# Kernel optimization log

Hardware: AMD Instinct MI355X
Metric: run time of the kernel (lower is better)

The kernel has to match this reference:

```python
import jax, jax.numpy as jnp
import numpy as np

BN_EPS = 1e-5

def setup_inputs() -> dict:
    key = jax.random.key(0)
    ks = jax.random.split(key, 6)
    B, C, N = 8, 256, 4096
    da = C // 4
    return {
        "x": jax.random.normal(ks[0], (B, C, N), dtype=jnp.float32),
        "Wq": jax.random.normal(ks[1], (da, C), dtype=jnp.float32) * (C ** -0.5),
        "Wk": jax.random.normal(ks[2], (da, C), dtype=jnp.float32) * (C ** -0.5),
        "Wv": jax.random.normal(ks[3], (C, C), dtype=jnp.float32) * (C ** -0.5),
        "Wp": jax.random.normal(ks[4], (C, C), dtype=jnp.float32) * (C ** -0.5),
        "bn_gamma": jnp.ones((C,), dtype=jnp.float32),
        "bn_beta": jnp.zeros((C,), dtype=jnp.float32),
        "bn_mean": jnp.zeros((C,), dtype=jnp.float32),
        "bn_var": jnp.ones((C,), dtype=jnp.float32),
    }

def reference(x, Wq, Wk, Wv, Wp, bn_gamma, bn_beta, bn_mean, bn_var):
    # x: [B, C, N]; 1x1 Conv1d == channel matmul
    q = jnp.einsum('bcn,dc->bnd', x, Wq)          # [B, N, da]
    k = jnp.einsum('bcn,dc->bdn', x, Wk)          # [B, da, N]
    v = jnp.einsum('bcn,dc->bnd', x, Wv)          # [B, N, C]
    energy = jnp.einsum('bnd,bdm->bnm', q, k)     # [B, N, N]
    # offset-attention double normalization: softmax over dim=1 (rows), then L1 over dim=-1
    attn = jax.nn.softmax(energy, axis=1)
    attn = attn / (1e-9 + attn.sum(axis=-1, keepdims=True))
    fsa = jnp.einsum('bnm,bmc->bcn', attn, v)     # [B, C, N]
    y = x - fsa
    h = jnp.einsum('bcn,dc->bdn', y, Wp)          # 1x1 conv of LBR
    # BatchNorm1d (inference-mode with running stats)
    inv = bn_gamma / jnp.sqrt(bn_var + BN_EPS)
    h = h * inv[None, :, None] + (bn_beta - bn_mean * inv)[None, :, None]
    return jax.nn.relu(h) + x
```

## Files before the change

kernel.cpp:

```cpp
#include <hip/hip_runtime.h>
#include <math.h>

#define BD 8
#define CD 256
#define ND 4096
#define DA 64

typedef __attribute__((ext_vector_type(8))) short short8v;
typedef __attribute__((ext_vector_type(4))) float float4v;

static __device__ __forceinline__ float4v mfma16(short8v a, short8v b, float4v c) {
  return __builtin_amdgcn_mfma_f32_16x16x32_bf16(a, b, c, 0, 0, 0);
}
static __device__ __forceinline__ unsigned short f2bf(float f) {
  union { float f; unsigned int u; } v; v.f = f;
  return (unsigned short)((v.u + 0x7fffu + ((v.u >> 16) & 1u)) >> 16);
}
static __device__ __forceinline__ float bf2f(unsigned short h) {
  union { unsigned int u; float f; } v; v.u = (unsigned int)h << 16;
  return v.f;
}
static __device__ __forceinline__ int sw(int row, int c8) {
  return row * 64 + (((c8) ^ (row & 7)) << 3);
}
typedef const __attribute__((address_space(1))) unsigned int g_u32;
typedef __attribute__((address_space(3))) unsigned int l_u32;
static __device__ __forceinline__ void gld16(const void* g, void* l) {
  __builtin_amdgcn_global_load_lds((g_u32*)g, (l_u32*)l, 16, 0, 0);
}

__global__ __launch_bounds__(256) void k_prep(const float* __restrict__ x,
                                              unsigned short* __restrict__ xTh,
                                              unsigned short* __restrict__ xTl) {
  const int n0 = blockIdx.x * 64, c0 = blockIdx.y * 64, b = blockIdx.z;
  __shared__ float Xs[64][68];
  const int tid = threadIdx.x;
  const int r0 = tid >> 4, col4 = (tid & 15) * 4;
#pragma unroll
  for (int j = 0; j < 4; ++j) {
    int r = r0 + j * 16;
    *(float4*)&Xs[r][col4] =
        *(const float4*)&x[((size_t)(b * CD + c0 + r)) * ND + n0 + col4];
  }
  __syncthreads();
  const int n = tid >> 2, cg = (tid & 3) * 16;
  unsigned short h[16], l[16];
#pragma unroll
  for (int j = 0; j < 16; ++j) {
    float v = Xs[cg + j][n];
    h[j] = f2bf(v);
    l[j] = f2bf(v - bf2f(h[j]));
  }
  size_t o = ((size_t)b * ND + n0 + n) * CD + c0 + cg;
#pragma unroll
  for (int j = 0; j < 4; ++j) {
    *(ushort4*)&xTh[o + j * 4] = *(ushort4*)&h[j * 4];
    *(ushort4*)&xTl[o + j * 4] = *(ushort4*)&l[j * 4];
  }
}

__global__ void k_prepW(const float* __restrict__ Wq, const float* __restrict__ Wk,
                        const float* __restrict__ Wv, const float* __restrict__ Wp,
                        unsigned short* Wch, unsigned short* Wcl,
                        unsigned short* Wph, unsigned short* Wpl) {
  int i = blockIdx.x * 256 + threadIdx.x;
  int row = i >> 6, c4 = (i & 63) * 4;
  const float* src; unsigned short *dh, *dl; int r, drow;
  if (row < 64)       { src = Wq; r = row;       dh = Wch; dl = Wcl; drow = row; }
  else if (row < 128) { src = Wk; r = row - 64;  dh = Wch; dl = Wcl; drow = row; }
  else if (row < 384) { src = Wv; r = row - 128; dh = Wch; dl = Wcl; drow = row; }
  else                { src = Wp; r = row - 384; dh = Wph; dl = Wpl; drow = row - 384; }
  float4 f = *(const float4*)&src[(size_t)r * 256 + c4];
  ushort4 hh, ll;
  hh.x = f2bf(f.x); hh.y = f2bf(f.y); hh.z = f2bf(f.z); hh.w = f2bf(f.w);
  ll.x = f2bf(f.x - bf2f(hh.x)); ll.y = f2bf(f.y - bf2f(hh.y));
  ll.z = f2bf(f.z - bf2f(hh.z)); ll.w = f2bf(f.w - bf2f(hh.w));
  *(ushort4*)&dh[(size_t)drow * 256 + c4] = hh;
  *(ushort4*)&dl[(size_t)drow * 256 + c4] = ll;
}

__global__ __launch_bounds__(512) void k_proj(
    const unsigned short* __restrict__ xTh, const unsigned short* __restrict__ xTl,
    const unsigned short* __restrict__ Wch, const unsigned short* __restrict__ Wcl,
    unsigned short* __restrict__ qh, unsigned short* __restrict__ kh,
    unsigned short* __restrict__ kl, unsigned short* __restrict__ vT) {
  const int n0 = blockIdx.x * 128, b = blockIdx.y;
  const int tid = threadIdx.x, w = tid >> 6, lane = tid & 63, lq = lane & 15,
            quad = lane >> 4;
  __shared__ __align__(16) unsigned short xs[2][2][128][40];
  float4v O[24];
#pragma unroll
  for (int t = 0; t < 24; ++t) O[t] = (float4v){0.f, 0.f, 0.f, 0.f};

  const int srow = tid >> 2, sc4 = tid & 3;
  uint4 rh, rl;
  auto load_slice = [&](int ks) {
    size_t a = ((size_t)b * ND + n0 + srow) * CD + ks * 32 + sc4 * 8;
    rh = *(const uint4*)(xTh + a);
    rl = *(const uint4*)(xTl + a);
  };
  auto write_slice = [&](int buf) {
    *(uint4*)&xs[buf][0][srow][sc4 * 8] = rh;
    *(uint4*)&xs[buf][1][srow][sc4 * 8] = rl;
  };
  load_slice(0); write_slice(0);
#pragma unroll 1
  for (int ks = 0; ks < 8; ++ks) {
    __syncthreads();
    if (ks < 7) load_slice(ks + 1);
    short8v bxh = *(const short8v*)&xs[ks & 1][0][w * 16 + lq][quad * 8];
    short8v bxl = *(const short8v*)&xs[ks & 1][1][w * 16 + lq][quad * 8];
#pragma unroll
    for (int t = 0; t < 24; ++t) {
      size_t a = (size_t)(t * 16 + lq) * CD + ks * 32 + quad * 8;
      short8v awh = *(const short8v*)(Wch + a);
      short8v awl = *(const short8v*)(Wcl + a);
      O[t] = mfma16(awh, bxh, O[t]);
      O[t] = mfma16(awl, bxh, O[t]);
      O[t] = mfma16(awh, bxl, O[t]);
    }
    if (ks < 7) write_slice((ks + 1) & 1);
  }
  const int n = n0 + w * 16 + lq;
#pragma unroll
  for (int t = 0; t < 24; ++t) {
    if (t < 4) {
      ushort4 hh;
      hh.x = f2bf(O[t][0]); hh.y = f2bf(O[t][1]);
      hh.z = f2bf(O[t][2]); hh.w = f2bf(O[t][3]);
      *(ushort4*)&qh[((size_t)b * ND + n) * DA + t * 16 + quad * 4] = hh;
    } else if (t < 8) {
      ushort4 hh, ll;
      hh.x = f2bf(O[t][0]); hh.y = f2bf(O[t][1]);
      hh.z = f2bf(O[t][2]); hh.w = f2bf(O[t][3]);
      ll.x = f2bf(O[t][0] - bf2f(hh.x)); ll.y = f2bf(O[t][1] - bf2f(hh.y));
      ll.z = f2bf(O[t][2] - bf2f(hh.z)); ll.w = f2bf(O[t][3] - bf2f(hh.w));
      size_t o = ((size_t)b * ND + n) * DA + (t - 4) * 16 + quad * 4;
      *(ushort4*)&kh[o] = hh;
      *(ushort4*)&kl[o] = ll;
    } else {
#pragma unroll
      for (int r = 0; r < 4; ++r) {
        int c = (t - 8) * 16 + quad * 4 + r;
        vT[((size_t)b * CD + c) * ND + n] = f2bf(O[t][r]);
      }
    }
  }
}

__global__ __launch_bounds__(512, 4) void k_colsum(
    const unsigned short* __restrict__ qh, const unsigned short* __restrict__ khp,
    const unsigned short* __restrict__ klp, float* __restrict__ Dp) {
  const int bid = blockIdx.x, b = bid & 7, half = (bid >> 3) & 1,
            m0 = (bid >> 4) * 128;
  const int nbase = half * 2048;
  const int tid = threadIdx.x, w = tid >> 6, lane = tid & 63, lq = lane & 15,
            quad = lane >> 4;
  const int mq = w & 3, nh = w >> 2;
  __shared__ __align__(16) unsigned short qbuf[3][4096];
  __shared__ float Cb[128];
  short8v bkh[2][2], bkl[2][2];
#pragma unroll
  for (int sub = 0; sub < 2; ++sub)
#pragma unroll
    for (int k = 0; k < 2; ++k) {
      size_t a = ((size_t)b * ND + m0 + mq * 32 + sub * 16 + lq) * DA + k * 32 + quad * 8;
      bkh[sub][k] = *(const short8v*)(khp + a);
      bkl[sub][k] = *(const short8v*)(klp + a);
    }
  const int srow = w * 8 + (lane >> 3), sck = lane & 7;
  auto stageQ = [&](int it, int qn) {
    const unsigned short* src = qh + ((size_t)b * ND + nbase + it * 64 + srow) * DA +
                                ((sck ^ (srow & 7)) << 3);
    gld16(src, &qbuf[qn][0] + (size_t)w * 512);
  };
  stageQ(0, 0);
  stageQ(1, 1);
  asm volatile("s_waitcnt vmcnt(1)\n\ts_barrier" ::: "memory");
  float cs0 = 0.f, cs1 = 0.f;
  float4v accP[2][2];
  int rc = 0, sc = 2;
#pragma unroll 1
  for (int i = 0; i < 32; ++i) {
    if (i < 30) { stageQ(i + 2, sc); sc = (sc + 1 == 3) ? 0 : sc + 1; }
    float4v accN[2][2];
#pragma unroll
    for (int s = 0; s < 2; ++s) {
      short8v ah[2];
#pragma unroll
      for (int k = 0; k < 2; ++k)
        ah[k] = *(const short8v*)&qbuf[rc][sw(nh * 32 + s * 16 + lq, k * 4 + quad)];
#pragma unroll
      for (int sub = 0; sub < 2; ++sub) {
        float4v acc = {0.f, 0.f, 0.f, 0.f};
#pragma unroll
        for (int k = 0; k < 2; ++k) {
          acc = mfma16(ah[k], bkh[sub][k], acc);
          acc = mfma16(ah[k], bkl[sub][k], acc);
        }
        accN[s][sub] = acc;
      }
    }
    if (i > 0) {
#pragma unroll
      for (int s = 0; s < 2; ++s)
#pragma unroll
        for (int sub = 0; sub < 2; ++sub) {
          float e0 = __expf(accP[s][sub][0]) + __expf(accP[s][sub][1]) +
                     __expf(accP[s][sub][2]) + __expf(accP[s][sub][3]);
          if (sub == 0) cs0 += e0; else cs1 += e0;
        }
    }
#pragma unroll
    for (int s = 0; s < 2; ++s)
#pragma unroll
      for (int sub = 0; sub < 2; ++sub) accP[s][sub] = accN[s][sub];
    rc = (rc + 1 == 3) ? 0 : rc + 1;
    if (i < 30)
      asm volatile("s_waitcnt vmcnt(1) lgkmcnt(0)\n\ts_barrier" ::: "memory");
    else
      asm volatile("s_waitcnt vmcnt(0) lgkmcnt(0)\n\ts_barrier" ::: "memory");
  }
#pragma unroll
  for (int s = 0; s < 2; ++s)
#pragma unroll
    for (int sub = 0; sub < 2; ++sub) {
      float e0 = __expf(accP[s][sub][0]) + __expf(accP[s][sub][1]) +
                 __expf(accP[s][sub][2]) + __expf(accP[s][sub][3]);
      if (sub == 0) cs0 += e0; else cs1 += e0;
    }
  cs0 += __shfl_down(cs0, 16); cs0 += __shfl_down(cs0, 32);
  cs1 += __shfl_down(cs1, 16); cs1 += __shfl_down(cs1, 32);
  if (nh == 0 && lane < 16) {
    Cb[mq * 32 + lane] = cs0;
    Cb[mq * 32 + 16 + lane] = cs1;
  }
  __syncthreads();
  if (nh == 1 && lane < 16) {
    float t0 = Cb[mq * 32 + lane] + cs0;
    float t1 = Cb[mq * 32 + 16 + lane] + cs1;
    size_t o = (size_t)half * (BD * ND) + (size_t)b * ND + m0 + mq * 32 + lane;
    Dp[o] = t0;
    Dp[o + 16] = t1;
  }
}

__global__ void k_rcp(const float* __restrict__ Dp, float* __restrict__ Drec) {
  int i = blockIdx.x * 256 + threadIdx.x;
  float4 a = *(const float4*)&Dp[(size_t)i * 4];
  float4 c = *(const float4*)&Dp[(size_t)(BD * ND) + (size_t)i * 4];
  float4 r;
  r.x = 1.f / (a.x + c.x); r.y = 1.f / (a.y + c.y);
  r.z = 1.f / (a.z + c.z); r.w = 1.f / (a.w + c.w);
  *(float4*)&Drec[(size_t)i * 4] = r;
}

__global__ __launch_bounds__(512, 2) void k_attn(
    const unsigned short* __restrict__ qh, const unsigned short* __restrict__ khp,
    const unsigned short* __restrict__ klp, const unsigned short* __restrict__ vT,
    const float* __restrict__ Drec, unsigned short* xhy,
    const unsigned short* __restrict__ xTl) {
  const int bid = blockIdx.x, b = bid & 7, n0 = (bid >> 3) * 128;
  const int tid = threadIdx.x, w = tid >> 6, lane = tid & 63, lq = lane & 15,
            quad = lane >> 4;
  const int nh = w & 1, mt = w >> 1;
  __shared__ __align__(16) unsigned short vbuf[3][16384];
  __shared__ __align__(16) unsigned short Pb[2][8192];
  __shared__ float Sb4[4][128];

  short8v aq[4][2];
#pragma unroll
  for (int s = 0; s < 4; ++s)
#pragma unroll
    for (int k = 0; k < 2; ++k)
      aq[s][k] = *(const short8v*)(qh + ((size_t)b * ND + n0 + nh * 64 + s * 16 + lq) * DA +
                                   k * 32 + quad * 8);
  float4v O[4][4];
#pragma unroll
  for (int ct = 0; ct < 4; ++ct)
#pragma unroll
    for (int s = 0; s < 4; ++s) O[ct][s] = (float4v){0.f, 0.f, 0.f, 0.f};
  float rs[4] = {0.f, 0.f, 0.f, 0.f};

  auto stageV = [&](int mtile, int vn) {
    unsigned short* base = &vbuf[vn][0];
#pragma unroll
    for (int j = 0; j < 4; ++j) {
      int cidx = tid + j * 512;
      int row = cidx >> 3, ckpos = cidx & 7;
      const unsigned short* src =
          vT + ((size_t)b * CD + row) * ND + mtile * 64 + ((ckpos ^ (row & 7)) << 3);
      gld16(src, base + (size_t)(w * 64 + j * 512) * 8);
    }
  };
  short8v kc[4];
  auto kload = [&](int mtile) {
#pragma unroll
    for (int k = 0; k < 2; ++k) {
      size_t a = ((size_t)b * ND + mtile * 64 + mt * 16 + lq) * DA + k * 32 + quad * 8;
      kc[k * 2 + 0] = *(const short8v*)(khp + a);
      kc[k * 2 + 1] = *(const short8v*)(klp + a);
    }
  };
  auto doPV = [&](const unsigned short* Pc, const unsigned short* vc) {
#pragma unroll
    for (int ks = 0; ks < 2; ++ks) {
      short8v ap[4];
#pragma unroll
      for (int s = 0; s < 4; ++s)
        ap[s] = *(const short8v*)&Pc[sw(nh * 64 + s * 16 + lq, ks * 4 + quad)];
#pragma unroll
      for (int ct = 0; ct < 4; ++ct) {
        const int trow = (mt * 4 + ct) * 16 + lq;
        short8v bv = *(const short8v*)&vc[sw(trow, ks * 4 + quad)];
#pragma unroll
        for (int s = 0; s < 4; ++s) O[ct][s] = mfma16(bv, ap[s], O[ct][s]);
      }
    }
  };
  auto eMFMA = [&](float4v* dst) {
#pragma unroll
    for (int s = 0; s < 4; ++s) {
      float4v acc = {0.f, 0.f, 0.f, 0.f};
#pragma unroll
      for (int k = 0; k < 2; ++k) {
        acc = mfma16(kc[k * 2 + 0], aq[s][k], acc);
        acc = mfma16(kc[k * 2 + 1], aq[s][k], acc);
      }
      dst[s] = acc;
    }
  };

  float4 drc4, drn4;
  stageV(0, 0);
  kload(0);
  drc4 = *(const float4*)&Drec[(size_t)b * ND + mt * 16 + quad * 4];
  float4v accP[4];
  eMFMA(accP);

  int vs = 1, vp = 0;
#pragma unroll 1
  for (int i = 0; i < 64; ++i) {
    if (i > 0) {
      doPV(&Pb[(i - 1) & 1][0], &vbuf[vp][0]);
      vp = (vp + 1 == 3) ? 0 : vp + 1;
    }
    if (i < 63) {
      kload(i + 1);
      drn4 = *(const float4*)&Drec[(size_t)b * ND + (i + 1) * 64 + mt * 16 + quad * 4];
      stageV(i + 1, vs);
      vs = (vs + 1 == 3) ? 0 : vs + 1;
    }
    unsigned short* Pcur = &Pb[i & 1][0];
#pragma unroll
    for (int s = 0; s < 4; ++s) {
      float p0 = __expf(accP[s][0]) * drc4.x;
      float p1 = __expf(accP[s][1]) * drc4.y;
      float p2 = __expf(accP[s][2]) * drc4.z;
      float p3 = __expf(accP[s][3]) * drc4.w;
      rs[s] += (p0 + p1) + (p2 + p3);
      unsigned int w0 =
          (__float_as_uint(p0) >> 16) | (__float_as_uint(p1) & 0xffff0000u);
      unsigned int w1 =
          (__float_as_uint(p2) >> 16) | (__float_as_uint(p3) & 0xffff0000u);
      const int nl = nh * 64 + s * 16 + lq;
      const int c8 = mt * 2 + (quad >> 1);
      uint2 wv; wv.x = w0; wv.y = w1;
      *(uint2*)&Pcur[nl * 64 + ((c8 ^ (nl & 7)) << 3) + ((quad & 1) << 2)] = wv;
    }
    if (i < 63) {
      eMFMA(accP);
      drc4 = drn4;
    }
    if (i < 63)
      asm volatile("s_waitcnt vmcnt(4) lgkmcnt(0)\n\ts_barrier" ::: "memory");
    else
      asm volatile("s_waitcnt vmcnt(0) lgkmcnt(0)\n\ts_barrier" ::: "memory");
  }
  doPV(&Pb[1][0], &vbuf[vp][0]);

#pragma unroll
  for (int s = 0; s < 4; ++s) {
    rs[s] += __shfl_xor(rs[s], 16);
    rs[s] += __shfl_xor(rs[s], 32);
  }
  if (lane < 16) {
#pragma unroll
    for (int s = 0; s < 4; ++s) Sb4[mt][nh * 64 + s * 16 + lane] = rs[s];
  }
  __syncthreads();
  float rsc[4];
#pragma unroll
  for (int s = 0; s < 4; ++s) {
    const int nloc = nh * 64 + s * 16 + lq;
    rsc[s] = 1.0f / (1e-9f + Sb4[0][nloc] + Sb4[1][nloc] + Sb4[2][nloc] + Sb4[3][nloc]);
  }
#pragma unroll
  for (int ct = 0; ct < 4; ++ct) {
    const int cb = (mt * 4 + ct) * 16 + quad * 4;
#pragma unroll
    for (int s = 0; s < 4; ++s) {
      const int n = n0 + nh * 64 + s * 16 + lq;
      const size_t off = ((size_t)b * ND + n) * CD + cb;
      ushort4 h4 = *(const ushort4*)&xhy[off];
      ushort4 l4 = *(const ushort4*)&xTl[off];
      ushort4 o4;
      o4.x = f2bf(bf2f(h4.x) + bf2f(l4.x) - O[ct][s][0] * rsc[s]);
      o4.y = f2bf(bf2f(h4.y) + bf2f(l4.y) - O[ct][s][1] * rsc[s]);
      o4.z = f2bf(bf2f(h4.z) + bf2f(l4.z) - O[ct][s][2] * rsc[s]);
      o4.w = f2bf(bf2f(h4.w) + bf2f(l4.w) - O[ct][s][3] * rsc[s]);
      *(ushort4*)&xhy[off] = o4;
    }
  }
}

__global__ __launch_bounds__(256) void k_final(const unsigned short* __restrict__ y,
                                               const unsigned short* __restrict__ Wpb,
                                               const float* __restrict__ x,
                                               const float* __restrict__ gamma,
                                               const float* __restrict__ beta,
                                               const float* __restrict__ mean,
                                               const float* __restrict__ var,
                                               float* __restrict__ out) {
  const int bid = blockIdx.x;
  const int b = bid & 7;
  const int rem = bid >> 3;
  const int n0 = (rem & 63) * 64;
  const int d0 = (rem >> 6) * 64;
  const int tid = threadIdx.x;
  const int wave = tid >> 6, lane = tid & 63, lq = lane & 15, quad = lane >> 4;
  const int dw = d0 + wave * 16;
  float4v O[4];
#pragma unroll
  for (int s = 0; s < 4; ++s) O[s] = (float4v){0.f, 0.f, 0.f, 0.f};
#pragma unroll
  for (int chh = 0; chh < 8; ++chh) {
    const size_t ab = (size_t)(dw + lq) * CD + chh * 32 + quad * 8;
    short8v a0 = *(const short8v*)(Wpb + ab);
#pragma unroll
    for (int s = 0; s < 4; ++s) {
      const size_t bb = ((size_t)b * ND + n0 + s * 16 + lq) * CD + chh * 32 + quad * 8;
      short8v bv = *(const short8v*)(y + bb);
      O[s] = mfma16(a0, bv, O[s]);
    }
  }
#pragma unroll
  for (int r = 0; r < 4; ++r) {
    const int d = dw + quad * 4 + r;
    const float inv  = gamma[d] / sqrtf(var[d] + 1e-5f);
    const float bias = beta[d] - mean[d] * inv;
#pragma unroll
    for (int s = 0; s < 4; ++s) {
      const int n = n0 + s * 16 + lq;
      const size_t oi = ((size_t)b * CD + d) * ND + n;
      out[oi] = fmaxf(O[s][r] * inv + bias, 0.f) + x[oi];
    }
  }
}

extern "C" void kernel_launch(void* const* d_in, const int* in_sizes, int n_in,
                              void* d_out, int out_size, void* d_ws, size_t ws_size,
                              hipStream_t stream) {
  const float* x     = (const float*)d_in[0];
  const float* Wq    = (const float*)d_in[1];
  const float* Wk    = (const float*)d_in[2];
  const float* Wv    = (const float*)d_in[3];
  const float* Wp    = (const float*)d_in[4];
  const float* gamma = (const float*)d_in[5];
  const float* beta  = (const float*)d_in[6];
  const float* mean  = (const float*)d_in[7];
  const float* var   = (const float*)d_in[8];
  float* out = (float*)d_out;

  char* wsp = (char*)d_ws;
  unsigned short* qhp = (unsigned short*)wsp; wsp += (size_t)BD * ND * DA * 2;
  unsigned short* khp = (unsigned short*)wsp; wsp += (size_t)BD * ND * DA * 2;
  unsigned short* klp = (unsigned short*)wsp; wsp += (size_t)BD * ND * DA * 2;
  unsigned short* vT  = (unsigned short*)wsp; wsp += (size_t)BD * CD * ND * 2;
  unsigned short* xTh = (unsigned short*)wsp; wsp += (size_t)BD * ND * CD * 2;
  unsigned short* xTl = (unsigned short*)wsp; wsp += (size_t)BD * ND * CD * 2;
  unsigned short* Wch = (unsigned short*)wsp; wsp += (size_t)384 * 256 * 2;
  unsigned short* Wcl = (unsigned short*)wsp; wsp += (size_t)384 * 256 * 2;
  unsigned short* Wph = (unsigned short*)wsp; wsp += (size_t)256 * 256 * 2;
  unsigned short* Wpl = (unsigned short*)wsp; wsp += (size_t)256 * 256 * 2;
  float* Drec = (float*)wsp; wsp += (size_t)BD * ND * 4;
  float* Dp   = (float*)wsp; wsp += (size_t)2 * BD * ND * 4;
  unsigned short* y = xTh;

  dim3 blk(256), blk5(512);
  k_prep<<<dim3(ND / 64, CD / 64, BD), blk, 0, stream>>>(x, xTh, xTl);
  k_prepW<<<dim3(160), blk, 0, stream>>>(Wq, Wk, Wv, Wp, Wch, Wcl, Wph, Wpl);
  k_proj<<<dim3(ND / 128, BD), blk5, 0, stream>>>(xTh, xTl, Wch, Wcl, qhp, khp,
                                                  klp, vT);
  k_colsum<<<dim3(512), blk5, 0, stream>>>(qhp, khp, klp, Dp);
  k_rcp<<<dim3(32), blk, 0, stream>>>(Dp, Drec);
  k_attn<<<dim3(256), blk5, 0, stream>>>(qhp, khp, klp, vT, Drec, y, xTl);
  k_final<<<dim3(2048), blk, 0, stream>>>(y, Wph, x, gamma, beta, mean, var, out);
}
```

Before: 437.1 us.

## Split attention over key halves with separate combine kernel

```diff
diff --git a/kernel.cpp b/kernel.cpp
--- a/kernel.cpp
+++ b/kernel.cpp
@@ -255,18 +255,19 @@
   *(float4*)&Drec[(size_t)i * 4] = r;
 }
 
-__global__ __launch_bounds__(512, 2) void k_attn(
+__global__ __launch_bounds__(512, 4) void k_attn(
     const unsigned short* __restrict__ qh, const unsigned short* __restrict__ khp,
     const unsigned short* __restrict__ klp, const unsigned short* __restrict__ vT,
-    const float* __restrict__ Drec, unsigned short* xhy,
-    const unsigned short* __restrict__ xTl) {
-  const int bid = blockIdx.x, b = bid & 7, n0 = (bid >> 3) * 128;
+    const float* __restrict__ Drec, float* __restrict__ Oa,
+    float* __restrict__ Rs) {
+  const int bid = blockIdx.x, b = bid & 7, nt = (bid >> 3) & 31, mhalf = bid >> 8;
+  const int n0 = nt * 128, mbase = mhalf * 32;
   const int tid = threadIdx.x, w = tid >> 6, lane = tid & 63, lq = lane & 15,
             quad = lane >> 4;
   const int nh = w & 1, mt = w >> 1;
-  __shared__ __align__(16) unsigned short vbuf[3][16384];
-  __shared__ __align__(16) unsigned short Pb[2][8192];
-  __shared__ float Sb4[4][128];
+  __shared__ __align__(16) unsigned char ldsraw[81920];
+  unsigned short* vbuf = (unsigned short*)ldsraw;
+  unsigned short* Pb = (unsigned short*)(ldsraw + 65536);
 
   short8v aq[4][2];
 #pragma unroll
@@ -282,33 +283,33 @@
     for (int s = 0; s < 4; ++s) O[ct][s] = (float4v){0.f, 0.f, 0.f, 0.f};
   float rs[4] = {0.f, 0.f, 0.f, 0.f};
 
-  auto stageV = [&](int mtile, int vn) {
-    unsigned short* base = &vbuf[vn][0];
+  auto stageV = [&](int it, int vn) {
+    unsigned short* base = vbuf + (size_t)vn * 16384;
 #pragma unroll
     for (int j = 0; j < 4; ++j) {
       int cidx = tid + j * 512;
       int row = cidx >> 3, ckpos = cidx & 7;
       const unsigned short* src =
-          vT + ((size_t)b * CD + row) * ND + mtile * 64 + ((ckpos ^ (row & 7)) << 3);
+          vT + ((size_t)b * CD + row) * ND + (mbase + it) * 64 + ((ckpos ^ (row & 7)) << 3);
       gld16(src, base + (size_t)(w * 64 + j * 512) * 8);
     }
   };
   short8v kc[4];
-  auto kload = [&](int mtile) {
+  auto kload = [&](int it) {
 #pragma unroll
     for (int k = 0; k < 2; ++k) {
-      size_t a = ((size_t)b * ND + mtile * 64 + mt * 16 + lq) * DA + k * 32 + quad * 8;
+      size_t a = ((size_t)b * ND + (mbase + it) * 64 + mt * 16 + lq) * DA + k * 32 + quad * 8;
       kc[k * 2 + 0] = *(const short8v*)(khp + a);
       kc[k * 2 + 1] = *(const short8v*)(klp + a);
     }
   };
-  auto doPV = [&](const unsigned short* Pc, const unsigned short* vc) {
+  auto doPV = [&](const unsigned short* vc) {
 #pragma unroll
     for (int ks = 0; ks < 2; ++ks) {
       short8v ap[4];
 #pragma unroll
       for (int s = 0; s < 4; ++s)
-        ap[s] = *(const short8v*)&Pc[sw(nh * 64 + s * 16 + lq, ks * 4 + quad)];
+        ap[s] = *(const short8v*)&Pb[sw(nh * 64 + s * 16 + lq, ks * 4 + quad)];
 #pragma unroll
       for (int ct = 0; ct < 4; ++ct) {
         const int trow = (mt * 4 + ct) * 16 + lq;
@@ -334,24 +335,17 @@
   float4 drc4, drn4;
   stageV(0, 0);
   kload(0);
-  drc4 = *(const float4*)&Drec[(size_t)b * ND + mt * 16 + quad * 4];
+  drc4 = *(const float4*)&Drec[(size_t)b * ND + (mbase + 0) * 64 + mt * 16 + quad * 4];
   float4v accP[4];
   eMFMA(accP);
 
-  int vs = 1, vp = 0;
 #pragma unroll 1
-  for (int i = 0; i < 64; ++i) {
-    if (i > 0) {
-      doPV(&Pb[(i - 1) & 1][0], &vbuf[vp][0]);
-      vp = (vp + 1 == 3) ? 0 : vp + 1;
-    }
-    if (i < 63) {
+  for (int i = 0; i < 32; ++i) {
+    if (i < 31) {
       kload(i + 1);
-      drn4 = *(const float4*)&Drec[(size_t)b * ND + (i + 1) * 64 + mt * 16 + quad * 4];
-      stageV(i + 1, vs);
-      vs = (vs + 1 == 3) ? 0 : vs + 1;
-    }
-    unsigned short* Pcur = &Pb[i & 1][0];
+      drn4 = *(const float4*)&Drec[(size_t)b * ND + (mbase + i + 1) * 64 + mt * 16 + quad * 4];
+      stageV(i + 1, (i + 1) & 1);
+    }
 #pragma unroll
     for (int s = 0; s < 4; ++s) {
       float p0 = __expf(accP[s][0]) * drc4.x;
@@ -366,52 +360,75 @@
       const int nl = nh * 64 + s * 16 + lq;
       const int c8 = mt * 2 + (quad >> 1);
       uint2 wv; wv.x = w0; wv.y = w1;
-      *(uint2*)&Pcur[nl * 64 + ((c8 ^ (nl & 7)) << 3) + ((quad & 1) << 2)] = wv;
-    }
-    if (i < 63) {
+      *(uint2*)&Pb[nl * 64 + ((c8 ^ (nl & 7)) << 3) + ((quad & 1) << 2)] = wv;
+    }
+    if (i < 31) {
       eMFMA(accP);
       drc4 = drn4;
     }
-    if (i < 63)
+    if (i < 31)
       asm volatile("s_waitcnt vmcnt(4) lgkmcnt(0)\n\ts_barrier" ::: "memory");
     else
       asm volatile("s_waitcnt vmcnt(0) lgkmcnt(0)\n\ts_barrier" ::: "memory");
-  }
-  doPV(&Pb[1][0], &vbuf[vp][0]);
+    doPV(vbuf + (size_t)(i & 1) * 16384);
+    if (i < 31)
+      asm volatile("s_waitcnt lgkmcnt(0)\n\ts_barrier" ::: "memory");
+  }
 
 #pragma unroll
   for (int s = 0; s < 4; ++s) {
     rs[s] += __shfl_xor(rs[s], 16);
     rs[s] += __shfl_xor(rs[s], 32);
   }
+  __syncthreads();
+  float* Sb = (float*)Pb;
   if (lane < 16) {
 #pragma unroll
-    for (int s = 0; s < 4; ++s) Sb4[mt][nh * 64 + s * 16 + lane] = rs[s];
+    for (int s = 0; s < 4; ++s) Sb[mt * 128 + nh * 64 + s * 16 + lane] = rs[s];
   }
   __syncthreads();
-  float rsc[4];
-#pragma unroll
-  for (int s = 0; s < 4; ++s) {
-    const int nloc = nh * 64 + s * 16 + lq;
-    rsc[s] = 1.0f / (1e-9f + Sb4[0][nloc] + Sb4[1][nloc] + Sb4[2][nloc] + Sb4[3][nloc]);
+  if (mt == 0 && lane < 16) {
+#pragma unroll
+    for (int s = 0; s < 4; ++s) {
+      const int nl = nh * 64 + s * 16 + lane;
+      float tot = Sb[nl] + Sb[128 + nl] + Sb[256 + nl] + Sb[384 + nl];
+      Rs[((size_t)mhalf * BD + b) * ND + n0 + nl] = tot;
+    }
   }
 #pragma unroll
   for (int ct = 0; ct < 4; ++ct) {
-    const int cb = (mt * 4 + ct) * 16 + quad * 4;
 #pragma unroll
     for (int s = 0; s < 4; ++s) {
       const int n = n0 + nh * 64 + s * 16 + lq;
-      const size_t off = ((size_t)b * ND + n) * CD + cb;
-      ushort4 h4 = *(const ushort4*)&xhy[off];
-      ushort4 l4 = *(const ushort4*)&xTl[off];
-      ushort4 o4;
-      o4.x = f2bf(bf2f(h4.x) + bf2f(l4.x) - O[ct][s][0] * rsc[s]);
-      o4.y = f2bf(bf2f(h4.y) + bf2f(l4.y) - O[ct][s][1] * rsc[s]);
-      o4.z = f2bf(bf2f(h4.z) + bf2f(l4.z) - O[ct][s][2] * rsc[s]);
-      o4.w = f2bf(bf2f(h4.w) + bf2f(l4.w) - O[ct][s][3] * rsc[s]);
-      *(ushort4*)&xhy[off] = o4;
-    }
-  }
+      const int c = (mt * 4 + ct) * 16 + quad * 4;
+      float4 v;
+      v.x = O[ct][s][0]; v.y = O[ct][s][1]; v.z = O[ct][s][2]; v.w = O[ct][s][3];
+      *(float4*)&Oa[(((size_t)mhalf * BD + b) * ND + n) * CD + c] = v;
+    }
+  }
+}
+
+__global__ __launch_bounds__(256) void k_comb(const float* __restrict__ Oa,
+                                              const float* __restrict__ Rs,
+                                              unsigned short* __restrict__ xhy,
+                                              const unsigned short* __restrict__ xTl) {
+  const int idx = blockIdx.x * 256 + threadIdx.x;
+  const int c4 = (idx & 63) * 4;
+  const int n = (idx >> 6) & (ND - 1);
+  const int b = idx >> 18;
+  const size_t bn = (size_t)b * ND + n;
+  float4 a = *(const float4*)&Oa[bn * CD + c4];
+  float4 c = *(const float4*)&Oa[((size_t)BD * ND + bn) * CD + c4];
+  const float rsc = 1.0f / (1e-9f + Rs[bn] + Rs[(size_t)BD * ND + bn]);
+  const size_t off = bn * CD + c4;
+  ushort4 h4 = *(const ushort4*)&xhy[off];
+  ushort4 l4 = *(const ushort4*)&xTl[off];
+  ushort4 o4;
+  o4.x = f2bf(bf2f(h4.x) + bf2f(l4.x) - (a.x + c.x) * rsc);
+  o4.y = f2bf(bf2f(h4.y) + bf2f(l4.y) - (a.y + c.y) * rsc);
+  o4.z = f2bf(bf2f(h4.z) + bf2f(l4.z) - (a.z + c.z) * rsc);
+  o4.w = f2bf(bf2f(h4.w) + bf2f(l4.w) - (a.w + c.w) * rsc);
+  *(ushort4*)&xhy[off] = o4;
 }
 
 __global__ __launch_bounds__(256) void k_final(const unsigned short* __restrict__ y,
@@ -485,6 +502,8 @@
   unsigned short* Wpl = (unsigned short*)wsp; wsp += (size_t)256 * 256 * 2;
   float* Drec = (float*)wsp; wsp += (size_t)BD * ND * 4;
   float* Dp   = (float*)wsp; wsp += (size_t)2 * BD * ND * 4;
+  float* Rs   = (float*)wsp; wsp += (size_t)2 * BD * ND * 4;
+  float* Oa   = (float*)wsp; wsp += (size_t)2 * BD * ND * CD * 4;
   unsigned short* y = xTh;
 
   dim3 blk(256), blk5(512);
@@ -494,6 +513,7 @@
                                                   klp, vT);
   k_colsum<<<dim3(512), blk5, 0, stream>>>(qhp, khp, klp, Dp);
   k_rcp<<<dim3(32), blk, 0, stream>>>(Dp, Drec);
-  k_attn<<<dim3(256), blk5, 0, stream>>>(qhp, khp, klp, vT, Drec, y, xTl);
+  k_attn<<<dim3(512), blk5, 0, stream>>>(qhp, khp, klp, vT, Drec, Oa, Rs);
+  k_comb<<<dim3(8192), blk, 0, stream>>>(Oa, Rs, y, xTl);
   k_final<<<dim3(2048), blk, 0, stream>>>(y, Wph, x, gamma, beta, mean, var, out);
 }
```

Result: slower. 794.8 us (+81.9%).
